# Performance work log

Hardware: AMD Instinct MI355X
Metric: run time of the kernel (lower is better)

## Reference

```python
import jax, jax.numpy as jnp
import numpy as np

LEAK = 0.95
THRESHOLD = 1.0
RESCALE = 2.0


def _xavier_uniform(key, shape, gain=2.0):
    fan_out, fan_in = shape
    bound = gain * np.sqrt(6.0 / (fan_in + fan_out))
    return jax.random.uniform(key, shape, jnp.float32, -bound, bound)


def setup_inputs() -> dict:
    key = jax.random.key(0)
    k_inp, k_w1, k_w2 = jax.random.split(key, 3)
    inp = jax.random.normal(k_inp, (8192, 784), jnp.float32)
    w1 = _xavier_uniform(k_w1, (800, 784))   # fc1.weight
    w2 = _xavier_uniform(k_w2, (10, 800))    # fc2.weight
    return {"inp": inp, "w1": w1, "w2": w2, "num_steps": 25}


@jax.custom_vjp
def spike_fn(x):
    return (x > 0).astype(x.dtype)

def _spike_fwd(x):
    return spike_fn(x), x

def _spike_bwd(x, g):
    # grad = g * 0.3 * relu(1 - |x|)  (surrogate BP)
    return (g * 0.3 * jnp.maximum(1.0 - jnp.abs(x), 0.0),)

spike_fn.defvjp(_spike_fwd, _spike_bwd)


def poisson_gen(key, inp):
    r = jax.random.uniform(key, inp.shape, inp.dtype)
    temp = (r * RESCALE <= jnp.abs(inp)).astype(inp.dtype) * jnp.sign(inp)
    return 0.5 * (temp + 1.0)


def reference(inp, w1, w2, num_steps):
    batch = inp.shape[0]
    x = inp.reshape(batch, -1)
    keys = jax.random.split(jax.random.key(42), num_steps)

    def step(carry, key):
        mem1, mem2 = carry
        sp = poisson_gen(key, x)                    # [B, 784]
        mem1 = LEAK * mem1 + (1.0 - LEAK) * (sp @ w1.T)  # [B, 800]
        mem_thr = mem1 / THRESHOLD - 1.0
        out = spike_fn(mem_thr)
        rst = jnp.where(mem_thr > 0, THRESHOLD, 0.0)
        mem1 = mem1 - jax.lax.stop_gradient(rst)
        mem2 = mem2 + out @ w2.T                    # [B, 10]
        return (mem1, mem2), None

    init = (jnp.zeros((batch, 800), x.dtype), jnp.zeros((batch, 10), x.dtype))
    (_, mem2), _ = jax.lax.scan(step, init, keys)
    return mem2 / num_steps
```

## Files before the change

### kernel.cpp

```cpp
#include <hip/hip_runtime.h>
#include <cstdint>

__host__ __device__ inline uint32_t tf_rotl32(uint32_t x, uint32_t r) {
  return (x << r) | (x >> (32u - r));
}

__host__ __device__ inline void threefry2x32(uint32_t k0, uint32_t k1,
                                             uint32_t x0, uint32_t x1,
                                             uint32_t* o0, uint32_t* o1) {
  uint32_t ks0 = k0, ks1 = k1, ks2 = k0 ^ k1 ^ 0x1BD11BDAu;
  x0 += ks0; x1 += ks1;
#define TF_R(r) { x0 += x1; x1 = tf_rotl32(x1, r); x1 ^= x0; }
  TF_R(13) TF_R(15) TF_R(26) TF_R(6)
  x0 += ks1; x1 += ks2 + 1u;
  TF_R(17) TF_R(29) TF_R(16) TF_R(24)
  x0 += ks2; x1 += ks0 + 2u;
  TF_R(13) TF_R(15) TF_R(26) TF_R(6)
  x0 += ks0; x1 += ks1 + 3u;
  TF_R(17) TF_R(29) TF_R(16) TF_R(24)
  x0 += ks1; x1 += ks2 + 4u;
  TF_R(13) TF_R(15) TF_R(26) TF_R(6)
  x0 += ks2; x1 += ks0 + 5u;
#undef TF_R
  *o0 = x0; *o1 = x1;
}

#define BSZ   8192
#define KIN   784
#define HID   800
#define NOUT  10
#define NSTEP 25

#define PANEL1 264
#define PANEL2 528

__global__ __launch_bounds__(256) void enc_kernel(const float* __restrict__ inp,
                                                  uint8_t* __restrict__ enc,
                                                  uint32_t k0, uint32_t k1) {
  int j = blockIdx.x * blockDim.x + threadIdx.x;
  if (j >= BSZ * KIN) return;
  uint32_t o0, o1;
  threefry2x32(k0, k1, 0u, (uint32_t)j, &o0, &o1);
  uint32_t bits = o0 ^ o1;
  float r = __uint_as_float((bits >> 9) | 0x3f800000u) - 1.0f;
  float x = inp[j];
  bool cond = (2.0f * r <= fabsf(x));
  int s = (x > 0.0f) ? 1 : ((x < 0.0f) ? -1 : 0);
  enc[j] = (uint8_t)(1 + (cond ? s : 0));
}

#define BM 128
#define BN 32
#define BK 16

__global__ __launch_bounds__(256) void gemm_kernel(const uint8_t* __restrict__ enc,
                                                   const float* __restrict__ w1,
                                                   float* __restrict__ g) {
  __shared__ float As[BK][BM];
  __shared__ float Bs[BK][BN];
  const int m0 = blockIdx.x * BM;
  const int n0 = blockIdx.y * BN;
  const int t  = threadIdx.x;
  const int tn = t % 8;
  const int tm = t / 8;
  const int arow  = t / 2;
  const int akofs = (t % 2) * 8;
  const int brow  = t / 8;
  const int bkofs = (t % 8) * 2;

  float acc[4][4] = {};
  float tot[4][4];

  for (int k0 = 0; k0 < KIN; k0 += BK) {
    {
      const uint8_t* src = enc + (size_t)(m0 + arow) * KIN + k0 + akofs;
      union { uint2 u; uint8_t b[8]; } v;
      v.u = *(const uint2*)src;
#pragma unroll
      for (int i = 0; i < 8; i++) As[akofs + i][arow] = (float)v.b[i];
    }
    {
      const float* src = w1 + (size_t)(n0 + brow) * KIN + k0 + bkofs;
      float2 v = *(const float2*)src;
      Bs[bkofs][brow]     = v.x;
      Bs[bkofs + 1][brow] = v.y;
    }
    __syncthreads();
#pragma unroll
    for (int kk = 0; kk < BK; kk++) {
      const int kglob = k0 + kk;
      if (kglob == PANEL1) {
#pragma unroll
        for (int mi = 0; mi < 4; mi++)
#pragma unroll
          for (int ni = 0; ni < 4; ni++) { tot[mi][ni] = acc[mi][ni]; acc[mi][ni] = 0.0f; }
      } else if (kglob == PANEL2) {
#pragma unroll
        for (int mi = 0; mi < 4; mi++)
#pragma unroll
          for (int ni = 0; ni < 4; ni++) { tot[mi][ni] = __fadd_rn(tot[mi][ni], acc[mi][ni]); acc[mi][ni] = 0.0f; }
      }
      float a[4], b[4];
#pragma unroll
      for (int i = 0; i < 4; i++) a[i] = As[kk][tm * 4 + i];
#pragma unroll
      for (int i = 0; i < 4; i++) b[i] = Bs[kk][tn * 4 + i];
#pragma unroll
      for (int mi = 0; mi < 4; mi++)
#pragma unroll
        for (int ni = 0; ni < 4; ni++)
          acc[mi][ni] = __builtin_fmaf(a[mi], b[ni], acc[mi][ni]);
    }
    __syncthreads();
  }
#pragma unroll
  for (int mi = 0; mi < 4; mi++) {
    float* dst = g + (size_t)(m0 + tm * 4 + mi) * HID + n0 + tn * 4;
#pragma unroll
    for (int ni = 0; ni < 4; ni++)
      dst[ni] = __fmul_rn(0.5f, __fadd_rn(tot[mi][ni], acc[mi][ni]));
  }
}

__global__ __launch_bounds__(256) void update_kernel(const float* __restrict__ g,
                                                     float* __restrict__ mem1,
                                                     const float* __restrict__ w2,
                                                     float* __restrict__ mem2) {
  __shared__ float w2s[NOUT * HID];
  for (int i = threadIdx.x; i < NOUT * HID; i += 256) w2s[i] = w2[i];
  __syncthreads();

  const int wave = threadIdx.x / 64;
  const int lane = threadIdx.x % 64;
  const int b = blockIdx.x * 4 + wave;

  const float* grow = g + (size_t)b * HID;
  float* mrow = mem1 + (size_t)b * HID;

  float acc[NOUT];
#pragma unroll
  for (int i = 0; i < NOUT; i++) acc[i] = 0.0f;

  for (int j = lane; j < HID; j += 64) {
    float m = __fadd_rn(__fmul_rn(0.95f, mrow[j]), __fmul_rn(0.05f, grow[j]));
    bool spike = __fadd_rn(m, -1.0f) > 0.0f;
    mrow[j] = spike ? __fadd_rn(m, -1.0f) : m;
    if (spike) {
#pragma unroll
      for (int i = 0; i < NOUT; i++) acc[i] += w2s[i * HID + j];
    }
  }
#pragma unroll
  for (int i = 0; i < NOUT; i++) {
    float v = acc[i];
    for (int off = 32; off > 0; off >>= 1) v += __shfl_down(v, off);
    if (lane == 0) mem2[(size_t)b * NOUT + i] += v;
  }
}

__global__ __launch_bounds__(256) void finalize_kernel(const float* __restrict__ mem2,
                                                       const int* __restrict__ ns,
                                                       float* __restrict__ out) {
  int i = blockIdx.x * blockDim.x + threadIdx.x;
  if (i < BSZ * NOUT) out[i] = mem2[i] / (float)(*ns);
}

extern "C" void kernel_launch(void* const* d_in, const int* in_sizes, int n_in,
                              void* d_out, int out_size, void* d_ws, size_t ws_size,
                              hipStream_t stream) {
  const float* inp = (const float*)d_in[0];
  const float* w1  = (const float*)d_in[1];
  const float* w2  = (const float*)d_in[2];
  const int*   dns = (const int*)d_in[3];
  float* out = (float*)d_out;

  char* ws = (char*)d_ws;
  size_t off = 0;
  uint8_t* enc = (uint8_t*)(ws + off);  off += (size_t)BSZ * KIN;
  off = (off + 255) & ~(size_t)255;
  float* g    = (float*)(ws + off);     off += (size_t)BSZ * HID * 4;
  float* mem1 = (float*)(ws + off);     off += (size_t)BSZ * HID * 4;
  float* mem2 = (float*)(ws + off);     off += (size_t)BSZ * NOUT * 4;

  (void)hipMemsetAsync(mem1, 0, (size_t)BSZ * HID * 4, stream);
  (void)hipMemsetAsync(mem2, 0, (size_t)BSZ * NOUT * 4, stream);

  uint32_t keys[NSTEP][2];
  for (int t = 0; t < NSTEP; t++)
    threefry2x32(0u, 42u, 0u, (uint32_t)t, &keys[t][0], &keys[t][1]);

  const int n_elem = BSZ * KIN;
  for (int t = 0; t < NSTEP; t++) {
    enc_kernel<<<(n_elem + 255) / 256, 256, 0, stream>>>(inp, enc, keys[t][0], keys[t][1]);
    gemm_kernel<<<dim3(BSZ / BM, HID / BN), 256, 0, stream>>>(enc, w1, g);
    update_kernel<<<BSZ / 4, 256, 0, stream>>>(g, mem1, w2, mem2);
  }
  finalize_kernel<<<(BSZ * NOUT + 255) / 256, 256, 0, stream>>>(mem2, dns, out);
}
```

Before: 4.792 ms.

## Store encoded bytes packed in LDS and raise GEMM per-thread tile to 8x4

The GEMM now keeps the encoded inputs as packed uint8 in shared memory, transposing them with byte-permute instructions, and converts them to float only at use. The block shrinks to 128 threads, each computing an 8x4 output tile, and B loads, LDS reads and output stores are widened to float4. The aim is less LDS traffic and footprint plus more FMAs per shared-memory load. In exchange each thread uses more registers and does extra byte-unpack ALU work in the inner loop.

```diff
diff --git a/kernel.cpp b/kernel.cpp
--- a/kernel.cpp
+++ b/kernel.cpp
@@ -53,37 +53,53 @@
 #define BN 32
 #define BK 16
 
-__global__ __launch_bounds__(256) void gemm_kernel(const uint8_t* __restrict__ enc,
+__device__ __forceinline__ float cvt_ub(uint32_t x, int i) {
+  return (float)((x >> (8 * i)) & 0xffu);
+}
+
+__global__ __launch_bounds__(128) void gemm_kernel(const uint8_t* __restrict__ enc,
                                                    const float* __restrict__ w1,
                                                    float* __restrict__ g) {
-  __shared__ float As[BK][BM];
+  __shared__ uint32_t As[BK][BM / 4];
   __shared__ float Bs[BK][BN];
   const int m0 = blockIdx.x * BM;
   const int n0 = blockIdx.y * BN;
   const int t  = threadIdx.x;
+
+  const int tm = t / 8;
   const int tn = t % 8;
-  const int tm = t / 8;
-  const int arow  = t / 2;
-  const int akofs = (t % 2) * 8;
-  const int brow  = t / 8;
-  const int bkofs = (t % 8) * 2;
-
-  float acc[4][4] = {};
-  float tot[4][4];
+
+  const int ar0 = (t % 32) * 4;
+  const int ak0 = (t / 32) * 4;
+
+  const int brow = t % 32;
+  const int bk0  = (t / 32) * 4;
+
+  float acc[8][4] = {};
+  float tot[8][4];
 
   for (int k0 = 0; k0 < KIN; k0 += BK) {
     {
-      const uint8_t* src = enc + (size_t)(m0 + arow) * KIN + k0 + akofs;
-      union { uint2 u; uint8_t b[8]; } v;
-      v.u = *(const uint2*)src;
-#pragma unroll
-      for (int i = 0; i < 8; i++) As[akofs + i][arow] = (float)v.b[i];
+      uint32_t r0 = *(const uint32_t*)(enc + (size_t)(m0 + ar0 + 0) * KIN + k0 + ak0);
+      uint32_t r1 = *(const uint32_t*)(enc + (size_t)(m0 + ar0 + 1) * KIN + k0 + ak0);
+      uint32_t r2 = *(const uint32_t*)(enc + (size_t)(m0 + ar0 + 2) * KIN + k0 + ak0);
+      uint32_t r3 = *(const uint32_t*)(enc + (size_t)(m0 + ar0 + 3) * KIN + k0 + ak0);
+      uint32_t a01  = __builtin_amdgcn_perm(r1, r0, 0x05010400u);
+      uint32_t a01h = __builtin_amdgcn_perm(r1, r0, 0x07030602u);
+      uint32_t a23  = __builtin_amdgcn_perm(r3, r2, 0x05010400u);
+      uint32_t a23h = __builtin_amdgcn_perm(r3, r2, 0x07030602u);
+      As[ak0 + 0][ar0 >> 2] = __builtin_amdgcn_perm(a23,  a01,  0x05040100u);
+      As[ak0 + 1][ar0 >> 2] = __builtin_amdgcn_perm(a23,  a01,  0x07060302u);
+      As[ak0 + 2][ar0 >> 2] = __builtin_amdgcn_perm(a23h, a01h, 0x05040100u);
+      As[ak0 + 3][ar0 >> 2] = __builtin_amdgcn_perm(a23h, a01h, 0x07060302u);
     }
     {
-      const float* src = w1 + (size_t)(n0 + brow) * KIN + k0 + bkofs;
-      float2 v = *(const float2*)src;
-      Bs[bkofs][brow]     = v.x;
-      Bs[bkofs + 1][brow] = v.y;
+      const float* src = w1 + (size_t)(n0 + brow) * KIN + k0 + bk0;
+      float4 v = *(const float4*)src;
+      Bs[bk0 + 0][brow] = v.x;
+      Bs[bk0 + 1][brow] = v.y;
+      Bs[bk0 + 2][brow] = v.z;
+      Bs[bk0 + 3][brow] = v.w;
     }
     __syncthreads();
 #pragma unroll
@@ -91,22 +107,29 @@
       const int kglob = k0 + kk;
       if (kglob == PANEL1) {
 #pragma unroll
-        for (int mi = 0; mi < 4; mi++)
+        for (int mi = 0; mi < 8; mi++)
 #pragma unroll
           for (int ni = 0; ni < 4; ni++) { tot[mi][ni] = acc[mi][ni]; acc[mi][ni] = 0.0f; }
       } else if (kglob == PANEL2) {
 #pragma unroll
-        for (int mi = 0; mi < 4; mi++)
+        for (int mi = 0; mi < 8; mi++)
 #pragma unroll
           for (int ni = 0; ni < 4; ni++) { tot[mi][ni] = __fadd_rn(tot[mi][ni], acc[mi][ni]); acc[mi][ni] = 0.0f; }
       }
-      float a[4], b[4];
-#pragma unroll
-      for (int i = 0; i < 4; i++) a[i] = As[kk][tm * 4 + i];
-#pragma unroll
-      for (int i = 0; i < 4; i++) b[i] = Bs[kk][tn * 4 + i];
-#pragma unroll
-      for (int mi = 0; mi < 4; mi++)
+      uint2 av = *(const uint2*)&As[kk][tm * 2];
+      float a[8];
+      a[0] = cvt_ub(av.x, 0);
+      a[1] = cvt_ub(av.x, 1);
+      a[2] = cvt_ub(av.x, 2);
+      a[3] = cvt_ub(av.x, 3);
+      a[4] = cvt_ub(av.y, 0);
+      a[5] = cvt_ub(av.y, 1);
+      a[6] = cvt_ub(av.y, 2);
+      a[7] = cvt_ub(av.y, 3);
+      float4 bv = *(const float4*)&Bs[kk][tn * 4];
+      float b[4] = {bv.x, bv.y, bv.z, bv.w};
+#pragma unroll
+      for (int mi = 0; mi < 8; mi++)
 #pragma unroll
         for (int ni = 0; ni < 4; ni++)
           acc[mi][ni] = __builtin_fmaf(a[mi], b[ni], acc[mi][ni]);
@@ -114,11 +137,14 @@
     __syncthreads();
   }
 #pragma unroll
-  for (int mi = 0; mi < 4; mi++) {
-    float* dst = g + (size_t)(m0 + tm * 4 + mi) * HID + n0 + tn * 4;
-#pragma unroll
-    for (int ni = 0; ni < 4; ni++)
-      dst[ni] = __fmul_rn(0.5f, __fadd_rn(tot[mi][ni], acc[mi][ni]));
+  for (int mi = 0; mi < 8; mi++) {
+    float* dst = g + (size_t)(m0 + tm * 8 + mi) * HID + n0 + tn * 4;
+    float4 o;
+    o.x = __fmul_rn(0.5f, __fadd_rn(tot[mi][0], acc[mi][0]));
+    o.y = __fmul_rn(0.5f, __fadd_rn(tot[mi][1], acc[mi][1]));
+    o.z = __fmul_rn(0.5f, __fadd_rn(tot[mi][2], acc[mi][2]));
+    o.w = __fmul_rn(0.5f, __fadd_rn(tot[mi][3], acc[mi][3]));
+    *(float4*)dst = o;
   }
 }
 
@@ -192,7 +218,7 @@
   const int n_elem = BSZ * KIN;
   for (int t = 0; t < NSTEP; t++) {
     enc_kernel<<<(n_elem + 255) / 256, 256, 0, stream>>>(inp, enc, keys[t][0], keys[t][1]);
-    gemm_kernel<<<dim3(BSZ / BM, HID / BN), 256, 0, stream>>>(enc, w1, g);
+    gemm_kernel<<<dim3(BSZ / BM, HID / BN), 128, 0, stream>>>(enc, w1, g);
     update_kernel<<<BSZ / 4, 256, 0, stream>>>(g, mem1, w2, mem2);
   }
   finalize_kernel<<<(BSZ * NOUT + 255) / 256, 256, 0, stream>>>(mem2, dns, out);
```

Result: slower. 6.142 ms (+28.2%).

## Double-buffer GEMM shared tiles and store encoded spikes as packed bytes

Applied to the files above, without the earlier changes.

The GEMM now prefetches the next K tile into registers while computing on the current one, using two shared-memory buffers so each tile needs only one barrier. The A operand stays packed as uint8 in shared memory, transposed with byte-permute instructions, and is converted to float at use time. B reads and output stores are vectorised to float4. This is meant to hide global-load latency and cut LDS traffic, at the cost of more registers and extra per-element conversion ALU work.

```diff
diff --git a/kernel.cpp b/kernel.cpp
--- a/kernel.cpp
+++ b/kernel.cpp
@@ -52,43 +52,80 @@
 #define BM 128
 #define BN 32
 #define BK 16
+#define NTILE (KIN / BK)
+
+__device__ __forceinline__ float cvt_ub(uint32_t x, int i) {
+  return (float)((x >> (8 * i)) & 0xffu);
+}
 
 __global__ __launch_bounds__(256) void gemm_kernel(const uint8_t* __restrict__ enc,
                                                    const float* __restrict__ w1,
                                                    float* __restrict__ g) {
-  __shared__ float As[BK][BM];
-  __shared__ float Bs[BK][BN];
+  __shared__ uint32_t As[2][BK][BM / 4];
+  __shared__ float    Bs[2][BK][BN];
   const int m0 = blockIdx.x * BM;
   const int n0 = blockIdx.y * BN;
   const int t  = threadIdx.x;
+
+  const int tm = t / 8;
   const int tn = t % 8;
-  const int tm = t / 8;
-  const int arow  = t / 2;
-  const int akofs = (t % 2) * 8;
-  const int brow  = t / 8;
-  const int bkofs = (t % 8) * 2;
+
+  const bool isA = (t < 128);
+  const int u    = t & 127;
+  const int ar0  = (u & 31) * 4;
+  const int ak0  = (u >> 5) * 4;
+  const int brow = u & 31;
+  const int bk0  = (u >> 5) * 4;
+
+  const uint8_t* aptr = enc + (size_t)(m0 + ar0) * KIN + ak0;
+  const float*   bptr = w1 + (size_t)(n0 + brow) * KIN + bk0;
+
+  uint32_t rA0, rA1, rA2, rA3;
+  float4 rB;
 
   float acc[4][4] = {};
   float tot[4][4];
 
-  for (int k0 = 0; k0 < KIN; k0 += BK) {
-    {
-      const uint8_t* src = enc + (size_t)(m0 + arow) * KIN + k0 + akofs;
-      union { uint2 u; uint8_t b[8]; } v;
-      v.u = *(const uint2*)src;
-#pragma unroll
-      for (int i = 0; i < 8; i++) As[akofs + i][arow] = (float)v.b[i];
-    }
-    {
-      const float* src = w1 + (size_t)(n0 + brow) * KIN + k0 + bkofs;
-      float2 v = *(const float2*)src;
-      Bs[bkofs][brow]     = v.x;
-      Bs[bkofs + 1][brow] = v.y;
-    }
-    __syncthreads();
+#define LOAD_TILE(K0G)                                               \
+  if (isA) {                                                         \
+    const uint8_t* ap = aptr + (K0G);                                \
+    rA0 = *(const uint32_t*)(ap + (size_t)0 * KIN);                  \
+    rA1 = *(const uint32_t*)(ap + (size_t)1 * KIN);                  \
+    rA2 = *(const uint32_t*)(ap + (size_t)2 * KIN);                  \
+    rA3 = *(const uint32_t*)(ap + (size_t)3 * KIN);                  \
+  } else {                                                           \
+    rB = *(const float4*)(bptr + (K0G));                             \
+  }
+
+#define STORE_TILE(P)                                                \
+  if (isA) {                                                         \
+    uint32_t a01  = __builtin_amdgcn_perm(rA1, rA0, 0x05010400u);    \
+    uint32_t a01h = __builtin_amdgcn_perm(rA1, rA0, 0x07030602u);    \
+    uint32_t a23  = __builtin_amdgcn_perm(rA3, rA2, 0x05010400u);    \
+    uint32_t a23h = __builtin_amdgcn_perm(rA3, rA2, 0x07030602u);    \
+    As[P][ak0 + 0][ar0 >> 2] = __builtin_amdgcn_perm(a23,  a01,  0x05040100u); \
+    As[P][ak0 + 1][ar0 >> 2] = __builtin_amdgcn_perm(a23,  a01,  0x07060302u); \
+    As[P][ak0 + 2][ar0 >> 2] = __builtin_amdgcn_perm(a23h, a01h, 0x05040100u); \
+    As[P][ak0 + 3][ar0 >> 2] = __builtin_amdgcn_perm(a23h, a01h, 0x07060302u); \
+  } else {                                                           \
+    Bs[P][bk0 + 0][brow] = rB.x;                                     \
+    Bs[P][bk0 + 1][brow] = rB.y;                                     \
+    Bs[P][bk0 + 2][brow] = rB.z;                                     \
+    Bs[P][bk0 + 3][brow] = rB.w;                                     \
+  }
+
+  LOAD_TILE(0)
+  STORE_TILE(0)
+  __syncthreads();
+
+  int p = 0;
+  for (int tile = 0; tile < NTILE; tile++) {
+    const int kbase = tile * BK;
+    const bool more = (tile + 1 < NTILE);
+    if (more) { LOAD_TILE(kbase + BK) }
 #pragma unroll
     for (int kk = 0; kk < BK; kk++) {
-      const int kglob = k0 + kk;
+      const int kglob = kbase + kk;
       if (kglob == PANEL1) {
 #pragma unroll
         for (int mi = 0; mi < 4; mi++)
@@ -100,25 +137,36 @@
 #pragma unroll
           for (int ni = 0; ni < 4; ni++) { tot[mi][ni] = __fadd_rn(tot[mi][ni], acc[mi][ni]); acc[mi][ni] = 0.0f; }
       }
-      float a[4], b[4];
-#pragma unroll
-      for (int i = 0; i < 4; i++) a[i] = As[kk][tm * 4 + i];
-#pragma unroll
-      for (int i = 0; i < 4; i++) b[i] = Bs[kk][tn * 4 + i];
+      uint32_t aw = As[p][kk][tm];
+      float a[4];
+      a[0] = cvt_ub(aw, 0);
+      a[1] = cvt_ub(aw, 1);
+      a[2] = cvt_ub(aw, 2);
+      a[3] = cvt_ub(aw, 3);
+      float4 bv = *(const float4*)&Bs[p][kk][tn * 4];
+      float b[4] = {bv.x, bv.y, bv.z, bv.w};
 #pragma unroll
       for (int mi = 0; mi < 4; mi++)
 #pragma unroll
         for (int ni = 0; ni < 4; ni++)
           acc[mi][ni] = __builtin_fmaf(a[mi], b[ni], acc[mi][ni]);
     }
+    if (more) { STORE_TILE(p ^ 1) }
     __syncthreads();
-  }
+    p ^= 1;
+  }
+#undef LOAD_TILE
+#undef STORE_TILE
+
 #pragma unroll
   for (int mi = 0; mi < 4; mi++) {
     float* dst = g + (size_t)(m0 + tm * 4 + mi) * HID + n0 + tn * 4;
-#pragma unroll
-    for (int ni = 0; ni < 4; ni++)
-      dst[ni] = __fmul_rn(0.5f, __fadd_rn(tot[mi][ni], acc[mi][ni]));
+    float4 o;
+    o.x = __fmul_rn(0.5f, __fadd_rn(tot[mi][0], acc[mi][0]));
+    o.y = __fmul_rn(0.5f, __fadd_rn(tot[mi][1], acc[mi][1]));
+    o.z = __fmul_rn(0.5f, __fadd_rn(tot[mi][2], acc[mi][2]));
+    o.w = __fmul_rn(0.5f, __fadd_rn(tot[mi][3], acc[mi][3]));
+    *(float4*)dst = o;
   }
 }
 
```

Result: no change. 4.800 ms (+0.2%).
